# Kernel tuning notes

Hardware: AMD Instinct MI355X
Metric: run time of the kernel (lower is better)

Reference implementation:

```python
import jax, jax.numpy as jnp
import numpy as np
import math

B, S, H = 2, 1024, 768
NH = 12
DH = H // NH  # 64


def _heads(t):
    # (B,S,H) -> (B,NH,S,DH)
    b, s, _ = t.shape
    return t.reshape(b, s, NH, DH).transpose(0, 2, 1, 3)


def _merge(t):
    # (B,NH,S,DH) -> (B,S,H)
    b, nh, s, dh = t.shape
    return t.transpose(0, 2, 1, 3).reshape(b, s, nh * dh)


def _forward(x, y, vq_w, vq_b, vk_w, vk_b, vv_w, vv_b,
             dq_w, dq_b, dk_w, dk_b, dv_w, dv_b,
             van_fc_w, van_fc_b, WD_w, d_theta_w, d_theta_b, WV_w,
             diff_fc_w, diff_fc_b, v_gamma_w, v_gamma_b,
             diff_out_w, diff_out_b, van_out_w, van_out_b,
             diff_fus_w, diff_fus_b, van_fus_w, van_fus_b,
             gate_w, nf_w, nf_b, nf_out_w, final_w, final_b):
    scale = 1.0 / math.sqrt(DH)

    # ---- Vanilla attention (dropout is eval-mode identity) ----
    q = _heads(x @ vq_w + vq_b)
    k = _heads(y @ vk_w + vk_b)
    v = _heads(y @ vv_w + vv_b)
    scores = jnp.einsum('bhid,bhjd->bhij', q, k) * scale
    probs = jax.nn.softmax(scores, axis=-1)
    van_vector = _merge(jnp.einsum('bhij,bhjd->bhid', probs, v))

    # ---- Differential attention ----
    # scores[b,h,i,j] = sum_d (q[b,h,i,d] - k[b,h,i,d]) / sqrt(DH)  (constant over j,
    # due to the module's broadcast indexing). Keep explicit softmax for exact math/vjp.
    dq = _heads(x @ dq_w + dq_b)
    dk = _heads(y @ dk_w + dk_b)
    dv = _heads(y @ dv_w + dv_b)
    s_row = (dq.sum(-1) - dk.sum(-1)) * scale  # (B,NH,S)
    d_scores = jnp.broadcast_to(s_row[..., None], s_row.shape + (s_row.shape[-1],))
    d_probs = jax.nn.softmax(d_scores, axis=-1)
    diff_vector = _merge(jnp.einsum('bhij,bhjd->bhid', d_probs, dv))

    # ---- Coupled gating (SoftMax over dim=1 == sequence axis) ----
    theta = jnp.tanh(jnp.concatenate((diff_vector @ WD_w, x_lin(van_vector, van_fc_w, van_fc_b)), axis=-1))
    d_theta = diff_vector * jax.nn.softmax(theta @ d_theta_w + d_theta_b, axis=1)
    gamma = jnp.tanh(jnp.concatenate((van_vector @ WV_w, d_theta @ diff_fc_w + diff_fc_b), axis=-1))
    a_gamma = van_vector * jax.nn.softmax(gamma @ v_gamma_w + v_gamma_b, axis=1)
    diff_out = jnp.tanh(jnp.concatenate((diff_vector, d_theta), axis=-1) @ diff_out_w + diff_out_b)
    van_out = jnp.tanh(jnp.concatenate((van_vector, a_gamma), axis=-1) @ van_out_w + van_out_b)
    diff_fusion = jnp.tanh(diff_out @ diff_fus_w + diff_fus_b)
    van_fusion = jnp.tanh(van_out @ van_fus_w + van_fus_b)
    gate = jax.nn.sigmoid(jnp.concatenate((diff_fusion, van_fusion), axis=-1) @ gate_w)  # (B,S,1)
    fusion = gate * van_fusion + (1.0 - gate) * diff_fusion
    nf = jax.nn.sigmoid(jnp.concatenate((van_vector, fusion @ nf_w + nf_b), axis=-1) @ nf_out_w)
    return nf * jnp.tanh(fusion @ final_w + final_b)


def x_lin(t, w, b):
    return t @ w + b


def setup_inputs() -> dict:
    key = jax.random.key(0)
    ks = iter(jax.random.split(key, 64))
    def w(*shape):
        return jax.random.normal(next(ks), shape, jnp.float32) * 0.02
    def b(n):
        return jnp.zeros((n,), jnp.float32)
    inp = {
        'x': jax.random.normal(next(ks), (B, S, H), jnp.float32),
        'y': jax.random.normal(next(ks), (B, S, H), jnp.float32),
        'vq_w': w(H, H), 'vq_b': b(H), 'vk_w': w(H, H), 'vk_b': b(H), 'vv_w': w(H, H), 'vv_b': b(H),
        'dq_w': w(H, H), 'dq_b': b(H), 'dk_w': w(H, H), 'dk_b': b(H), 'dv_w': w(H, H), 'dv_b': b(H),
        'van_fc_w': w(H, H), 'van_fc_b': b(H),
        'WD_w': w(H, H),
        'd_theta_w': w(2 * H, H), 'd_theta_b': b(H),
        'WV_w': w(H, H),
        'diff_fc_w': w(H, H), 'diff_fc_b': b(H),
        'v_gamma_w': w(2 * H, H), 'v_gamma_b': b(H),
        'diff_out_w': w(2 * H, H), 'diff_out_b': b(H),
        'van_out_w': w(2 * H, H), 'van_out_b': b(H),
        'diff_fus_w': w(H, H), 'diff_fus_b': b(H),
        'van_fus_w': w(H, H), 'van_fus_b': b(H),
        'gate_w': w(2 * H, 1),
        'nf_w': w(H, H), 'nf_b': b(H),
        'nf_out_w': w(2 * H, 1),
        'final_w': w(H, H), 'final_b': b(H),
    }
    return inp


def reference(x, y, vq_w, vq_b, vk_w, vk_b, vv_w, vv_b,
              dq_w, dq_b, dk_w, dk_b, dv_w, dv_b,
              van_fc_w, van_fc_b, WD_w, d_theta_w, d_theta_b, WV_w,
              diff_fc_w, diff_fc_b, v_gamma_w, v_gamma_b,
              diff_out_w, diff_out_b, van_out_w, van_out_b,
              diff_fus_w, diff_fus_b, van_fus_w, van_fus_b,
              gate_w, nf_w, nf_b, nf_out_w, final_w, final_b):
    return _forward(x, y, vq_w, vq_b, vk_w, vk_b, vv_w, vv_b,
                    dq_w, dq_b, dk_w, dk_b, dv_w, dv_b,
                    van_fc_w, van_fc_b, WD_w, d_theta_w, d_theta_b, WV_w,
                    diff_fc_w, diff_fc_b, v_gamma_w, v_gamma_b,
                    diff_out_w, diff_out_b, van_out_w, van_out_b,
                    diff_fus_w, diff_fus_b, van_fus_w, van_fus_b,
                    gate_w, nf_w, nf_b, nf_out_w, final_w, final_b)
```

## Files before the change

### kernel.cpp

```cpp
#include <hip/hip_runtime.h>
#include <hip/hip_bf16.h>
#include <math.h>

#define H 768
#define S 1024
#define BATCH 2
#define T 2048
#define TH ((size_t)T * H)

typedef unsigned short u16;
typedef __attribute__((ext_vector_type(8))) short short8;
typedef __attribute__((ext_vector_type(4))) float f32x4;

__device__ __forceinline__ u16 f2b(float f) {
  __hip_bfloat16 h = __float2bfloat16(f);
  return *reinterpret_cast<u16*>(&h);
}
__device__ __forceinline__ float b2f(u16 u) {
  __hip_bfloat16 h = *reinterpret_cast<__hip_bfloat16*>(&u);
  return __bfloat162float(h);
}
__device__ __forceinline__ void gload16(const u16* g, u16* lds) {
  __builtin_amdgcn_global_load_lds((const __attribute__((address_space(1))) void*)g,
                                   (__attribute__((address_space(3))) void*)lds, 16, 0, 0);
}

__global__ __launch_bounds__(256) void cvt2_k(const float* __restrict__ X, const float* __restrict__ Y,
                                              u16* __restrict__ OX, u16* __restrict__ OY) {
  const float* src = blockIdx.y ? Y : X;
  u16* dst = blockIdx.y ? OY : OX;
  int i = blockIdx.x * 256 + threadIdx.x;
  float4 a = ((const float4*)src)[2 * i];
  float4 b = ((const float4*)src)[2 * i + 1];
  u16 tmp[8] = {f2b(a.x), f2b(a.y), f2b(a.z), f2b(a.w), f2b(b.x), f2b(b.y), f2b(b.z), f2b(b.w)};
  ((uint4*)dst)[i] = *(uint4*)tmp;
}

struct WprepArgs {
  const float* src[14];
  unsigned dst[14];
  int ktiles[14];
  int tstart[15];
};
__global__ __launch_bounds__(256) void wprep_k(WprepArgs a, u16* __restrict__ wt) {
  __shared__ float sT[64][68];
  int blk = blockIdx.x;
  int mi = 0;
  while (blk >= a.tstart[mi + 1]) ++mi;
  int local = blk - a.tstart[mi];
  int kt = a.ktiles[mi];
  int tn = local / kt, tk = local % kt;
  int K = kt * 64;
  const float* W = a.src[mi];
  u16* D = wt + a.dst[mi];
  int t = threadIdx.x;
  int r = t >> 2, c = (t & 3) * 16;
  const float4* srcp = (const float4*)(W + ((size_t)(tk * 64 + r)) * H + tn * 64 + c);
  float4 v0 = srcp[0], v1 = srcp[1], v2 = srcp[2], v3 = srcp[3];
  *(float4*)&sT[r][c] = v0; *(float4*)&sT[r][c + 4] = v1;
  *(float4*)&sT[r][c + 8] = v2; *(float4*)&sT[r][c + 12] = v3;
  __syncthreads();
  int n = t >> 2, kk = (t & 3) * 16;
  u16 tmp[16];
  #pragma unroll
  for (int j = 0; j < 16; ++j) tmp[j] = f2b(sT[kk + j][n]);
  uint4* dst = (uint4*)(D + ((size_t)(tn * 64 + n)) * K + tk * 64 + kk);
  dst[0] = *(uint4*)&tmp[0];
  dst[1] = *(uint4*)&tmp[8];
}

__global__ __launch_bounds__(256) void meany1_k(const float* __restrict__ Y, float* __restrict__ part) {
  int blk = blockIdx.x;
  int b = blk / 24, r = blk % 24, cc = r / 8, sc = r % 8;
  int c = cc * 256 + threadIdx.x;
  const float* yp = Y + (size_t)b * S * H + (size_t)sc * 128 * H + c;
  float s = 0.f;
  for (int j = 0; j < 128; ++j) s += yp[(size_t)j * H];
  part[(sc * 2 + b) * H + c] = s;
}
__global__ __launch_bounds__(256) void meany2_k(const float* __restrict__ part, float* __restrict__ ybar) {
  int t = blockIdx.x * 256 + threadIdx.x;
  float s = 0.f;
  int b = t / H, c = t % H;
  #pragma unroll
  for (int sc = 0; sc < 8; ++sc) s += part[(sc * 2 + b) * H + c];
  ybar[t] = s * (1.0f / 1024.0f);
}

__global__ __launch_bounds__(256) void gemv_k(const float* __restrict__ A, const float* __restrict__ W,
                                              const float* __restrict__ bias, float* __restrict__ O, int act) {
  int gid = blockIdx.x * 4 + (threadIdx.x >> 6);
  int lane = threadIdx.x & 63;
  int b = gid / H, n = gid % H;
  const float* a = A + b * H;
  float s = 0.f;
  #pragma unroll
  for (int i = 0; i < 12; ++i) {
    int k = lane + 64 * i;
    s = fmaf(a[k], W[(size_t)k * H + n], s);
  }
  #pragma unroll
  for (int off = 32; off; off >>= 1) s += __shfl_xor(s, off);
  if (lane == 0) {
    if (bias) s += bias[n];
    if (act) s = tanhf(s);
    O[gid] = s;
  }
}

struct Reg {
  const u16 *A, *W, *A2, *W2;
  const float *bias, *perbatch;
  u16* Cb; u16* CbT; float* Cf; float* colPart;
  int ldw, ldw2;
};
struct GArgs { Reg r0, r1, r2; int act; };

__global__ __launch_bounds__(256) void bgemm_k(GArgs ga) {
  __shared__ u16 sA[3][64 * 64];
  __shared__ u16 sB[3][64 * 64];
  int t = threadIdx.x;
  int ri = blockIdx.x / 12;
  Reg R;
  if (ri == 0) R = ga.r0; else if (ri == 1) R = ga.r1; else R = ga.r2;
  int n0 = (blockIdx.x % 12) * 64;
  int m0 = blockIdx.y * 64;
  int w = t >> 6, l = t & 63, lr = l & 15, lg = l >> 4;
  int wr = (w >> 1) * 32, wc = (w & 1) * 32;

  f32x4 acc[2][2];
  #pragma unroll
  for (int i = 0; i < 2; ++i)
    #pragma unroll
    for (int j = 0; j < 2; ++j) acc[i][j] = (f32x4){0.f, 0.f, 0.f, 0.f};

  int NT = R.A2 ? 24 : 12;

  auto stage = [&](int ti) {
    int bi = ti % 3;
    const u16* Aq = (ti < 12) ? R.A : R.A2;
    const u16* Wq = (ti < 12) ? R.W : R.W2;
    int ldwq = (ti < 12) ? R.ldw : R.ldw2;
    int k0 = (ti % 12) * 64;
    #pragma unroll
    for (int ii = 0; ii < 2; ++ii) {
      int chunk = w * 128 + ii * 64 + l;
      int rr = chunk >> 3, c8 = chunk & 7;
      gload16(Aq + (size_t)(m0 + rr) * H + k0 + 8 * (c8 ^ (rr & 7)), &sA[bi][0] + (w * 128 + ii * 64) * 8);
      gload16(Wq + (size_t)(n0 + rr) * ldwq + k0 + 8 * (c8 ^ (rr & 7)), &sB[bi][0] + (w * 128 + ii * 64) * 8);
    }
  };

  stage(0);
  stage(1);
  for (int kt = 0; kt < NT; ++kt) {
    if (kt + 1 < NT) asm volatile("s_waitcnt vmcnt(4)" ::: "memory");
    else             asm volatile("s_waitcnt vmcnt(0)" ::: "memory");
    __builtin_amdgcn_s_barrier();
    if (kt + 2 < NT) stage(kt + 2);
    const u16* sAv = &sA[kt % 3][0];
    const u16* sBv = &sB[kt % 3][0];
    #pragma unroll
    for (int kh = 0; kh < 2; ++kh) {
      short8 af[2], bfr[2];
      #pragma unroll
      for (int mi = 0; mi < 2; ++mi) {
        int row = wr + 16 * mi + lr;
        af[mi] = *(const short8*)(sAv + row * 64 + 8 * ((4 * kh + lg) ^ (row & 7)));
      }
      #pragma unroll
      for (int ni = 0; ni < 2; ++ni) {
        int row = wc + 16 * ni + lr;
        bfr[ni] = *(const short8*)(sBv + row * 64 + 8 * ((4 * kh + lg) ^ (row & 7)));
      }
      #pragma unroll
      for (int mi = 0; mi < 2; ++mi)
        #pragma unroll
        for (int ni = 0; ni < 2; ++ni)
          acc[mi][ni] = __builtin_amdgcn_mfma_f32_16x16x32_bf16(af[mi], bfr[ni], acc[mi][ni], 0, 0, 0);
    }
  }

  float ps[2] = {0.f, 0.f};
  #pragma unroll
  for (int mi = 0; mi < 2; ++mi) {
    #pragma unroll
    for (int ni = 0; ni < 2; ++ni) {
      int col = n0 + wc + 16 * ni + lr;
      u16 tmp4[4];
      #pragma unroll
      for (int reg = 0; reg < 4; ++reg) {
        int row = m0 + wr + 16 * mi + lg * 4 + reg;
        int bb = row >> 10;
        float v = acc[mi][ni][reg];
        if (R.bias) v += R.bias[col];
        if (R.perbatch) v += R.perbatch[bb * H + col];
        if (ga.act) v = tanhf(v);
        tmp4[reg] = f2b(v);
        if (R.Cb) R.Cb[(size_t)row * H + col] = tmp4[reg];
        if (R.Cf) R.Cf[(size_t)row * H + col] = v;
        if (R.colPart) ps[ni] += __expf(b2f(tmp4[reg]));
      }
      if (R.CbT) {
        int row0 = m0 + wr + 16 * mi + lg * 4;
        int bb = row0 >> 10, tok = row0 & 1023, hh = col >> 6, dd = col & 63;
        *(unsigned long long*)&R.CbT[((size_t)((bb * 12 + hh) * 64 + dd)) * 1024 + tok] =
            *(unsigned long long*)tmp4;
      }
    }
  }
  if (R.colPart) {
    #pragma unroll
    for (int ni = 0; ni < 2; ++ni) {
      float p = ps[ni];
      p += __shfl_xor(p, 16);
      p += __shfl_xor(p, 32);
      if (lg == 0) {
        int col = n0 + wc + 16 * ni + lr;
        R.colPart[(size_t)(blockIdx.y * 2 + (wr >> 5)) * H + col] = p;
      }
    }
  }
}

__global__ __launch_bounds__(256) void mattn_k(
    const u16* __restrict__ Q, const u16* __restrict__ Kg,
    const u16* __restrict__ VT, u16* __restrict__ O)
{
  __shared__ u16 sK[3][64 * 64];
  __shared__ u16 sV[3][64 * 64];
  __shared__ u16 sQ[64 * 64];
  __shared__ u16 sP[4 * 16 * 64];
  int t = threadIdx.x;
  int w = t >> 6, l = t & 63, lr = l & 15, lg = l >> 4;
  int blk = blockIdx.x;
  int b = blk / 192; int rem = blk % 192; int h = rem / 16; int q0 = (rem % 16) * 64;

  #pragma unroll
  for (int i = 0; i < 2; ++i) {
    int id = t + i * 256; int r = id >> 3, c = id & 7;
    uint4 v = *(const uint4*)(Q + ((size_t)(b * 1024 + q0 + r)) * H + h * 64 + 8 * c);
    *(uint4*)(&sQ[0] + r * 64 + 8 * (c ^ (r & 7))) = v;
  }
  asm volatile("s_waitcnt lgkmcnt(0)" ::: "memory");

  auto stageKV = [&](int ti) {
    int bi = ti % 3;
    int kv0 = ti * 64;
    #pragma unroll
    for (int ii = 0; ii < 2; ++ii) {
      int chunk = w * 128 + ii * 64 + l;
      int rr = chunk >> 3, c8 = chunk & 7;
      gload16(Kg + ((size_t)(b * 1024 + kv0 + rr)) * H + h * 64 + 8 * (c8 ^ (rr & 7)),
              &sK[bi][0] + (w * 128 + ii * 64) * 8);
      gload16(VT + ((size_t)((b * 12 + h) * 64 + rr)) * 1024 + kv0 + 8 * (c8 ^ (rr & 7)),
              &sV[bi][0] + (w * 128 + ii * 64) * 8);
    }
  };

  f32x4 oacc[4];
  #pragma unroll
  for (int i = 0; i < 4; ++i) oacc[i] = (f32x4){0.f, 0.f, 0.f, 0.f};
  float lsum[4] = {0.f, 0.f, 0.f, 0.f};

  stageKV(0);
  stageKV(1);

  for (int kt = 0; kt < 16; ++kt) {
    if (kt + 1 < 16) asm volatile("s_waitcnt vmcnt(4)" ::: "memory");
    else             asm volatile("s_waitcnt vmcnt(0)" ::: "memory");
    __builtin_amdgcn_s_barrier();
    if (kt + 2 < 16) stageKV(kt + 2);
    const u16* sKv = &sK[kt % 3][0];
    const u16* sVv = &sV[kt % 3][0];

    f32x4 sacc[4];
    #pragma unroll
    for (int i = 0; i < 4; ++i) sacc[i] = (f32x4){0.f, 0.f, 0.f, 0.f};
    #pragma unroll
    for (int kh = 0; kh < 2; ++kh) {
      int qrow = 16 * w + lr;
      short8 qf = *(const short8*)(&sQ[0] + qrow * 64 + 8 * ((4 * kh + lg) ^ (qrow & 7)));
      #pragma unroll
      for (int ns = 0; ns < 4; ++ns) {
        int krow = 16 * ns + lr;
        short8 kf = *(const short8*)(sKv + krow * 64 + 8 * ((4 * kh + lg) ^ (krow & 7)));
        sacc[ns] = __builtin_amdgcn_mfma_f32_16x16x32_bf16(qf, kf, sacc[ns], 0, 0, 0);
      }
    }

    #pragma unroll
    for (int r = 0; r < 4; ++r) {
      int q = lg * 4 + r;
      #pragma unroll
      for (int ns = 0; ns < 4; ++ns) {
        float p = __expf(sacc[ns][r] * 0.125f);
        lsum[r] += p;
        int kv = 16 * ns + lr;
        unsigned byteoff = (unsigned)(w * 2048 + q * 128 + ((kv * 2) ^ ((q & 7) << 4)));
        *(u16*)((char*)sP + byteoff) = f2b(p);
      }
    }

    #pragma unroll
    for (int kh = 0; kh < 2; ++kh) {
      short8 pf = *(const short8*)((char*)sP + w * 2048 + lr * 128 + (((4 * kh + lg) << 4) ^ ((lr & 7) << 4)));
      #pragma unroll
      for (int ds = 0; ds < 4; ++ds) {
        int vrow = 16 * ds + lr;
        short8 vf = *(const short8*)(sVv + vrow * 64 + 8 * ((4 * kh + lg) ^ (vrow & 7)));
        oacc[ds] = __builtin_amdgcn_mfma_f32_16x16x32_bf16(pf, vf, oacc[ds], 0, 0, 0);
      }
    }
  }

  #pragma unroll
  for (int r = 0; r < 4; ++r) {
    #pragma unroll
    for (int off = 1; off < 16; off <<= 1) lsum[r] += __shfl_xor(lsum[r], off);
    float inv = 1.0f / lsum[r];
    int qrow = q0 + 16 * w + lg * 4 + r;
    #pragma unroll
    for (int ds = 0; ds < 4; ++ds) {
      int d = 16 * ds + lr;
      O[((size_t)(b * 1024 + qrow)) * H + h * 64 + d] = f2b(oacc[ds][r] * inv);
    }
  }
}

__global__ __launch_bounds__(256) void colsmA_k(
    const u16* __restrict__ Z, const float* __restrict__ part,
    const float* __restrict__ mulvec, const u16* __restrict__ mulmat, u16* __restrict__ O) {
  int blk = blockIdx.x;
  int b = blk >> 7, sc = blk & 127;
  int t = threadIdx.x;
  float s0 = 0.f, s1 = 0.f, s2 = 0.f;
  for (int i = b * 32; i < b * 32 + 32; ++i) {
    const float* pp = part + (size_t)i * H;
    s0 += pp[t]; s1 += pp[t + 256]; s2 += pp[t + 512];
  }
  float i0 = 1.0f / s0, i1 = 1.0f / s1, i2 = 1.0f / s2;
  size_t base = ((size_t)(b * 1024 + sc * 8)) * H;
  float m0 = 0.f, m1 = 0.f, m2 = 0.f;
  if (mulvec) { m0 = mulvec[b * H + t]; m1 = mulvec[b * H + t + 256]; m2 = mulvec[b * H + t + 512]; }
  #pragma unroll
  for (int j = 0; j < 8; ++j) {
    size_t row = base + (size_t)j * H;
    float e0 = __expf(b2f(Z[row + t]));
    float e1 = __expf(b2f(Z[row + t + 256]));
    float e2 = __expf(b2f(Z[row + t + 512]));
    float u0 = mulmat ? b2f(mulmat[row + t]) : m0;
    float u1 = mulmat ? b2f(mulmat[row + t + 256]) : m1;
    float u2 = mulmat ? b2f(mulmat[row + t + 512]) : m2;
    O[row + t] = f2b(u0 * e0 * i0);
    O[row + t + 256] = f2b(u1 * e1 * i1);
    O[row + t + 512] = f2b(u2 * e2 * i2);
  }
}

__global__ __launch_bounds__(256) void gatefuse_k(
    const u16* __restrict__ DF, const u16* __restrict__ VF,
    const float* __restrict__ GW, u16* __restrict__ FU)
{
  __shared__ float red[256];
  int tok = blockIdx.x;
  int t = threadIdx.x;
  const u16* df = DF + (size_t)tok * H;
  const u16* vf = VF + (size_t)tok * H;
  float dv[3], vv[3];
  float p = 0.f;
  #pragma unroll
  for (int i = 0; i < 3; ++i) {
    int c = t + i * 256;
    dv[i] = b2f(df[c]); vv[i] = b2f(vf[c]);
    p = fmaf(dv[i], GW[c], p);
    p = fmaf(vv[i], GW[H + c], p);
  }
  red[t] = p; __syncthreads();
  for (int st = 128; st; st >>= 1) { if (t < st) red[t] += red[t + st]; __syncthreads(); }
  float g = 1.0f / (1.0f + __expf(-red[0]));
  u16* fu = FU + (size_t)tok * H;
  #pragma unroll
  for (int i = 0; i < 3; ++i) {
    int c = t + i * 256;
    fu[c] = f2b(g * vv[i] + (1.0f - g) * dv[i]);
  }
}

__global__ __launch_bounds__(256) void nffinal_k(
    const u16* __restrict__ VAN, const float* __restrict__ NP,
    const float* __restrict__ NW, const float* __restrict__ FP,
    float* __restrict__ OUT)
{
  __shared__ float red[256];
  int tok = blockIdx.x;
  int t = threadIdx.x;
  const u16* va = VAN + (size_t)tok * H;
  const float* np = NP + (size_t)tok * H;
  float p = 0.f;
  #pragma unroll
  for (int i = 0; i < 3; ++i) {
    int c = t + i * 256;
    p = fmaf(b2f(va[c]), NW[c], p);
    p = fmaf(np[c], NW[H + c], p);
  }
  red[t] = p; __syncthreads();
  for (int st = 128; st; st >>= 1) { if (t < st) red[t] += red[t + st]; __syncthreads(); }
  float nf = 1.0f / (1.0f + __expf(-red[0]));
  const float* fp = FP + (size_t)tok * H;
  float* o = OUT + (size_t)tok * H;
  #pragma unroll
  for (int i = 0; i < 3; ++i) {
    int c = t + i * 256;
    o[c] = nf * tanhf(fp[c]);
  }
}

extern "C" void kernel_launch(void* const* d_in, const int* in_sizes, int n_in,
                              void* d_out, int out_size, void* d_ws, size_t ws_size,
                              hipStream_t stream) {
  const float* x        = (const float*)d_in[0];
  const float* y        = (const float*)d_in[1];
  const float* vq_w     = (const float*)d_in[2];
  const float* vq_b     = (const float*)d_in[3];
  const float* vk_w     = (const float*)d_in[4];
  const float* vk_b     = (const float*)d_in[5];
  const float* vv_w     = (const float*)d_in[6];
  const float* vv_b     = (const float*)d_in[7];
  const float* dv_w     = (const float*)d_in[12];
  const float* dv_b     = (const float*)d_in[13];
  const float* van_fc_w = (const float*)d_in[14];
  const float* van_fc_b = (const float*)d_in[15];
  const float* d_theta_w= (const float*)d_in[17];
  const float* WV_w     = (const float*)d_in[19];
  const float* diff_fc_w= (const float*)d_in[20];
  const float* diff_fc_b= (const float*)d_in[21];
  const float* v_gamma_w= (const float*)d_in[22];
  const float* diff_out_w=(const float*)d_in[24];
  const float* diff_out_b=(const float*)d_in[25];
  const float* van_out_w= (const float*)d_in[26];
  const float* van_out_b= (const float*)d_in[27];
  const float* diff_fus_w=(const float*)d_in[28];
  const float* diff_fus_b=(const float*)d_in[29];
  const float* van_fus_w= (const float*)d_in[30];
  const float* van_fus_b= (const float*)d_in[31];
  const float* gate_w   = (const float*)d_in[32];
  const float* nf_w     = (const float*)d_in[33];
  const float* nf_b     = (const float*)d_in[34];
  const float* nf_out_w = (const float*)d_in[35];
  const float* final_w  = (const float*)d_in[36];
  const float* final_b  = (const float*)d_in[37];
  float* out = (float*)d_out;

  u16* wt = (u16*)d_ws;
  const size_t HH_ = (size_t)H * H;
  const size_t HH2 = 2 * HH_;
  size_t woff[14];
  const float* wsrc[14] = {vq_w, vk_w, vv_w, van_fc_w, WV_w, diff_fc_w, diff_fus_w, van_fus_w,
                           nf_w, final_w, d_theta_w, v_gamma_w, diff_out_w, van_out_w};
  int wk[14] = {12,12,12,12,12,12,12,12,12,12, 24,24,24,24};
  size_t o = 0;
  for (int i = 0; i < 14; ++i) { woff[i] = o; o += (i < 10) ? HH_ : HH2; }
  u16* bufs = wt + o;
  u16* bX   = bufs + 0 * TH;
  u16* bY   = bufs + 1 * TH;
  u16* bQ   = bufs + 2 * TH;
  u16* bK   = bufs + 3 * TH;
  u16* bV   = bufs + 4 * TH;
  u16* bVT  = bufs + 5 * TH;
  u16* bVan = bufs + 6 * TH;
  float* F0 = (float*)(bufs + 7 * TH);
  float* F1 = F0 + TH;
  float* sm = F1 + TH;
  float* ybar  = sm;
  float* dvbar = sm + 1536;
  float* c2    = sm + 3072;
  float* part  = sm + 4608;
  float* colp  = sm + 4608 + 12288;

  WprepArgs wa;
  int ts = 0;
  for (int i = 0; i < 14; ++i) {
    wa.src[i] = wsrc[i];
    wa.dst[i] = (unsigned)woff[i];
    wa.ktiles[i] = wk[i];
    wa.tstart[i] = ts;
    ts += wk[i] * 12;
  }
  wa.tstart[14] = ts;
  wprep_k<<<ts, 256, 0, stream>>>(wa, wt);
  cvt2_k<<<dim3(TH / 8 / 256, 2), 256, 0, stream>>>(x, y, bX, bY);

  meany1_k<<<48, 256, 0, stream>>>(y, part);
  meany2_k<<<6, 256, 0, stream>>>(part, ybar);
  gemv_k<<<384, 256, 0, stream>>>(ybar, dv_w, dv_b, dvbar, 0);
  gemv_k<<<384, 256, 0, stream>>>(dvbar, diff_out_w, diff_out_b, c2, 0);

  const u16 *wt_vq = wt + woff[0], *wt_vk = wt + woff[1], *wt_vv = wt + woff[2],
            *wt_vanfc = wt + woff[3], *wt_WV = wt + woff[4], *wt_difffc = wt + woff[5],
            *wt_difffus = wt + woff[6], *wt_vanfus = wt + woff[7], *wt_nf = wt + woff[8],
            *wt_final = wt + woff[9], *wt_dtheta = wt + woff[10], *wt_vg = wt + woff[11],
            *wt_diffout = wt + woff[12], *wt_vanout = wt + woff[13];
  #define NO nullptr
  Reg RZ = {NO, NO, NO, NO, NO, NO, NO, NO, NO, NO, 0, 0};

  {
    GArgs g;
    g.r0 = {bX, wt_vq, NO, NO, vq_b, NO, bQ, NO, NO, NO, H, 0};
    g.r1 = {bY, wt_vk, NO, NO, vk_b, NO, bK, NO, NO, NO, H, 0};
    g.r2 = {bY, wt_vv, NO, NO, vv_b, NO, NO, bVT, NO, NO, H, 0};
    g.act = 0;
    bgemm_k<<<dim3(36, 32), 256, 0, stream>>>(g);
  }
  mattn_k<<<384, 256, 0, stream>>>(bQ, bK, bVT, bVan);

  {
    GArgs g;
    g.r0 = {bVan, wt_vanfc, NO, NO, van_fc_b, NO, bX, NO, NO, NO, H, 0};
    g.r1 = {bVan, wt_WV, NO, NO, NO, NO, bK, NO, NO, NO, H, 0};
    g.r2 = RZ;
    g.act = 1;
    bgemm_k<<<dim3(24, 32), 256, 0, stream>>>(g);
  }
  {
    GArgs g;
    g.r0 = {bX, wt_dtheta + H, NO, NO, NO, NO, bY, NO, NO, colp, 2 * H, 0};
    g.r1 = RZ; g.r2 = RZ;
    g.act = 0;
    bgemm_k<<<dim3(12, 32), 256, 0, stream>>>(g);
  }
  colsmA_k<<<256, 256, 0, stream>>>(bY, colp, dvbar, NO, bQ);
  {
    GArgs g;
    g.r0 = {bQ, wt_difffc, NO, NO, diff_fc_b, NO, bV, NO, NO, NO, H, 0};
    g.r1 = {bQ, wt_diffout + H, NO, NO, NO, c2, bY, NO, NO, NO, 2 * H, 0};
    g.r2 = RZ;
    g.act = 1;
    bgemm_k<<<dim3(24, 32), 256, 0, stream>>>(g);
  }
  {
    GArgs g;
    g.r0 = {bK, wt_vg, bV, wt_vg + H, NO, NO, bX, NO, NO, colp, 2 * H, 2 * H};
    g.r1 = RZ; g.r2 = RZ;
    g.act = 0;
    bgemm_k<<<dim3(12, 32), 256, 0, stream>>>(g);
  }
  colsmA_k<<<256, 256, 0, stream>>>(bX, colp, NO, bVan, bX);
  {
    GArgs g;
    g.r0 = {bVan, wt_vanout, bX, wt_vanout + H, van_out_b, NO, bK, NO, NO, NO, 2 * H, 2 * H};
    g.r1 = {bY, wt_difffus, NO, NO, diff_fus_b, NO, bQ, NO, NO, NO, H, 0};
    g.r2 = RZ;
    g.act = 1;
    bgemm_k<<<dim3(24, 32), 256, 0, stream>>>(g);
  }
  {
    GArgs g;
    g.r0 = {bK, wt_vanfus, NO, NO, van_fus_b, NO, bV, NO, NO, NO, H, 0};
    g.r1 = RZ; g.r2 = RZ;
    g.act = 1;
    bgemm_k<<<dim3(12, 32), 256, 0, stream>>>(g);
  }
  gatefuse_k<<<T, 256, 0, stream>>>(bQ, bV, gate_w, bY);
  {
    GArgs g;
    g.r0 = {bY, wt_nf, NO, NO, nf_b, NO, NO, NO, F0, NO, H, 0};
    g.r1 = {bY, wt_final, NO, NO, final_b, NO, NO, NO, F1, NO, H, 0};
    g.r2 = RZ;
    g.act = 0;
    bgemm_k<<<dim3(24, 32), 256, 0, stream>>>(g);
  }
  nffinal_k<<<T, 256, 0, stream>>>(bVan, F0, nf_out_w, F1, out);
}
```

Baseline: 232.9 us.

## Use 8 waves per GEMM block and keep Q fragments in registers in attention

The batched GEMM kernel moves from 4 waves (each computing a 32x32 subtile) to 8 waves (each computing a 16x32 subtile) per 64x64 output tile. Each thread now issues one async load per operand per stage, and the vmcnt waits and per-block column-partial indexing are adjusted to match, with colsm reading 64 partial rows per batch. This raises waves per block to hide latency, at the cost of less register-level reuse of B fragments. Separately, the attention kernel loads its Q fragments into registers once, after the KV prefetch is issued, instead of rereading them from LDS on every KV tile.

Result: faster. 226.3 us (-2.8%).

```diff
diff --git a/kernel.cpp b/kernel.cpp
--- a/kernel.cpp
+++ b/kernel.cpp
@@ -116,7 +116,7 @@
 };
 struct GArgs { Reg r0, r1, r2; int act; };
 
-__global__ __launch_bounds__(256) void bgemm_k(GArgs ga) {
+__global__ __launch_bounds__(512) void bgemm_k(GArgs ga) {
   __shared__ u16 sA[3][64 * 64];
   __shared__ u16 sB[3][64 * 64];
   int t = threadIdx.x;
@@ -126,13 +126,11 @@
   int n0 = (blockIdx.x % 12) * 64;
   int m0 = blockIdx.y * 64;
   int w = t >> 6, l = t & 63, lr = l & 15, lg = l >> 4;
-  int wr = (w >> 1) * 32, wc = (w & 1) * 32;
-
-  f32x4 acc[2][2];
-  #pragma unroll
-  for (int i = 0; i < 2; ++i)
-    #pragma unroll
-    for (int j = 0; j < 2; ++j) acc[i][j] = (f32x4){0.f, 0.f, 0.f, 0.f};
+  int wr = (w & 3) * 16, wc = (w >> 2) * 32;
+
+  f32x4 acc[2];
+  acc[0] = (f32x4){0.f, 0.f, 0.f, 0.f};
+  acc[1] = (f32x4){0.f, 0.f, 0.f, 0.f};
 
   int NT = R.A2 ? 24 : 12;
 
@@ -142,19 +140,15 @@
     const u16* Wq = (ti < 12) ? R.W : R.W2;
     int ldwq = (ti < 12) ? R.ldw : R.ldw2;
     int k0 = (ti % 12) * 64;
-    #pragma unroll
-    for (int ii = 0; ii < 2; ++ii) {
-      int chunk = w * 128 + ii * 64 + l;
-      int rr = chunk >> 3, c8 = chunk & 7;
-      gload16(Aq + (size_t)(m0 + rr) * H + k0 + 8 * (c8 ^ (rr & 7)), &sA[bi][0] + (w * 128 + ii * 64) * 8);
-      gload16(Wq + (size_t)(n0 + rr) * ldwq + k0 + 8 * (c8 ^ (rr & 7)), &sB[bi][0] + (w * 128 + ii * 64) * 8);
-    }
+    int rr = t >> 3, c8 = t & 7;
+    gload16(Aq + (size_t)(m0 + rr) * H + k0 + 8 * (c8 ^ (rr & 7)), &sA[bi][0] + t * 8);
+    gload16(Wq + (size_t)(n0 + rr) * ldwq + k0 + 8 * (c8 ^ (rr & 7)), &sB[bi][0] + t * 8);
   };
 
   stage(0);
   stage(1);
   for (int kt = 0; kt < NT; ++kt) {
-    if (kt + 1 < NT) asm volatile("s_waitcnt vmcnt(4)" ::: "memory");
+    if (kt + 1 < NT) asm volatile("s_waitcnt vmcnt(2)" ::: "memory");
     else             asm volatile("s_waitcnt vmcnt(0)" ::: "memory");
     __builtin_amdgcn_s_barrier();
     if (kt + 2 < NT) stage(kt + 2);
@@ -162,51 +156,40 @@
     const u16* sBv = &sB[kt % 3][0];
     #pragma unroll
     for (int kh = 0; kh < 2; ++kh) {
-      short8 af[2], bfr[2];
-      #pragma unroll
-      for (int mi = 0; mi < 2; ++mi) {
-        int row = wr + 16 * mi + lr;
-        af[mi] = *(const short8*)(sAv + row * 64 + 8 * ((4 * kh + lg) ^ (row & 7)));
-      }
+      int arow = wr + lr;
+      short8 af = *(const short8*)(sAv + arow * 64 + 8 * ((4 * kh + lg) ^ (arow & 7)));
       #pragma unroll
       for (int ni = 0; ni < 2; ++ni) {
-        int row = wc + 16 * ni + lr;
-        bfr[ni] = *(const short8*)(sBv + row * 64 + 8 * ((4 * kh + lg) ^ (row & 7)));
+        int brow = wc + 16 * ni + lr;
+        short8 bf = *(const short8*)(sBv + brow * 64 + 8 * ((4 * kh + lg) ^ (brow & 7)));
+        acc[ni] = __builtin_amdgcn_mfma_f32_16x16x32_bf16(af, bf, acc[ni], 0, 0, 0);
       }
-      #pragma unroll
-      for (int mi = 0; mi < 2; ++mi)
-        #pragma unroll
-        for (int ni = 0; ni < 2; ++ni)
-          acc[mi][ni] = __builtin_amdgcn_mfma_f32_16x16x32_bf16(af[mi], bfr[ni], acc[mi][ni], 0, 0, 0);
     }
   }
 
   float ps[2] = {0.f, 0.f};
   #pragma unroll
-  for (int mi = 0; mi < 2; ++mi) {
-    #pragma unroll
-    for (int ni = 0; ni < 2; ++ni) {
-      int col = n0 + wc + 16 * ni + lr;
-      u16 tmp4[4];
-      #pragma unroll
-      for (int reg = 0; reg < 4; ++reg) {
-        int row = m0 + wr + 16 * mi + lg * 4 + reg;
-        int bb = row >> 10;
-        float v = acc[mi][ni][reg];
-        if (R.bias) v += R.bias[col];
-        if (R.perbatch) v += R.perbatch[bb * H + col];
-        if (ga.act) v = tanhf(v);
-        tmp4[reg] = f2b(v);
-        if (R.Cb) R.Cb[(size_t)row * H + col] = tmp4[reg];
-        if (R.Cf) R.Cf[(size_t)row * H + col] = v;
-        if (R.colPart) ps[ni] += __expf(b2f(tmp4[reg]));
-      }
-      if (R.CbT) {
-        int row0 = m0 + wr + 16 * mi + lg * 4;
-        int bb = row0 >> 10, tok = row0 & 1023, hh = col >> 6, dd = col & 63;
-        *(unsigned long long*)&R.CbT[((size_t)((bb * 12 + hh) * 64 + dd)) * 1024 + tok] =
-            *(unsigned long long*)tmp4;
-      }
+  for (int ni = 0; ni < 2; ++ni) {
+    int col = n0 + wc + 16 * ni + lr;
+    u16 tmp4[4];
+    #pragma unroll
+    for (int reg = 0; reg < 4; ++reg) {
+      int row = m0 + wr + lg * 4 + reg;
+      int bb = row >> 10;
+      float v = acc[ni][reg];
+      if (R.bias) v += R.bias[col];
+      if (R.perbatch) v += R.perbatch[bb * H + col];
+      if (ga.act) v = tanhf(v);
+      tmp4[reg] = f2b(v);
+      if (R.Cb) R.Cb[(size_t)row * H + col] = tmp4[reg];
+      if (R.Cf) R.Cf[(size_t)row * H + col] = v;
+      if (R.colPart) ps[ni] += __expf(b2f(tmp4[reg]));
+    }
+    if (R.CbT) {
+      int row0 = m0 + wr + lg * 4;
+      int bb = row0 >> 10, tok = row0 & 1023, hh = col >> 6, dd = col & 63;
+      *(unsigned long long*)&R.CbT[((size_t)((bb * 12 + hh) * 64 + dd)) * 1024 + tok] =
+          *(unsigned long long*)tmp4;
     }
   }
   if (R.colPart) {
@@ -217,7 +200,7 @@
       p += __shfl_xor(p, 32);
       if (lg == 0) {
         int col = n0 + wc + 16 * ni + lr;
-        R.colPart[(size_t)(blockIdx.y * 2 + (wr >> 5)) * H + col] = p;
+        R.colPart[(size_t)(blockIdx.y * 4 + (w & 3)) * H + col] = p;
       }
     }
   }
@@ -242,7 +225,6 @@
     uint4 v = *(const uint4*)(Q + ((size_t)(b * 1024 + q0 + r)) * H + h * 64 + 8 * c);
     *(uint4*)(&sQ[0] + r * 64 + 8 * (c ^ (r & 7))) = v;
   }
-  asm volatile("s_waitcnt lgkmcnt(0)" ::: "memory");
 
   auto stageKV = [&](int ti) {
     int bi = ti % 3;
@@ -258,13 +240,21 @@
     }
   };
 
+  stageKV(0);
+  stageKV(1);
+  asm volatile("s_waitcnt lgkmcnt(0)" ::: "memory");
+  __builtin_amdgcn_s_barrier();
+  short8 qreg[2];
+  #pragma unroll
+  for (int kh = 0; kh < 2; ++kh) {
+    int qrow = 16 * w + lr;
+    qreg[kh] = *(const short8*)(&sQ[0] + qrow * 64 + 8 * ((4 * kh + lg) ^ (qrow & 7)));
+  }
+
   f32x4 oacc[4];
   #pragma unroll
   for (int i = 0; i < 4; ++i) oacc[i] = (f32x4){0.f, 0.f, 0.f, 0.f};
   float lsum[4] = {0.f, 0.f, 0.f, 0.f};
-
-  stageKV(0);
-  stageKV(1);
 
   for (int kt = 0; kt < 16; ++kt) {
     if (kt + 1 < 16) asm volatile("s_waitcnt vmcnt(4)" ::: "memory");
@@ -279,13 +269,11 @@
     for (int i = 0; i < 4; ++i) sacc[i] = (f32x4){0.f, 0.f, 0.f, 0.f};
     #pragma unroll
     for (int kh = 0; kh < 2; ++kh) {
-      int qrow = 16 * w + lr;
-      short8 qf = *(const short8*)(&sQ[0] + qrow * 64 + 8 * ((4 * kh + lg) ^ (qrow & 7)));
       #pragma unroll
       for (int ns = 0; ns < 4; ++ns) {
         int krow = 16 * ns + lr;
         short8 kf = *(const short8*)(sKv + krow * 64 + 8 * ((4 * kh + lg) ^ (krow & 7)));
-        sacc[ns] = __builtin_amdgcn_mfma_f32_16x16x32_bf16(qf, kf, sacc[ns], 0, 0, 0);
+        sacc[ns] = __builtin_amdgcn_mfma_f32_16x16x32_bf16(qreg[kh], kf, sacc[ns], 0, 0, 0);
       }
     }
 
@@ -335,7 +323,7 @@
   int b = blk >> 7, sc = blk & 127;
   int t = threadIdx.x;
   float s0 = 0.f, s1 = 0.f, s2 = 0.f;
-  for (int i = b * 32; i < b * 32 + 32; ++i) {
+  for (int i = b * 64; i < b * 64 + 64; ++i) {
     const float* pp = part + (size_t)i * H;
     s0 += pp[t]; s1 += pp[t + 256]; s2 += pp[t + 512];
   }
@@ -510,7 +498,7 @@
     g.r1 = {bY, wt_vk, NO, NO, vk_b, NO, bK, NO, NO, NO, H, 0};
     g.r2 = {bY, wt_vv, NO, NO, vv_b, NO, NO, bVT, NO, NO, H, 0};
     g.act = 0;
-    bgemm_k<<<dim3(36, 32), 256, 0, stream>>>(g);
+    bgemm_k<<<dim3(36, 32), 512, 0, stream>>>(g);
   }
   mattn_k<<<384, 256, 0, stream>>>(bQ, bK, bVT, bVan);
 
@@ -520,14 +508,14 @@
     g.r1 = {bVan, wt_WV, NO, NO, NO, NO, bK, NO, NO, NO, H, 0};
     g.r2 = RZ;
     g.act = 1;
-    bgemm_k<<<dim3(24, 32), 256, 0, stream>>>(g);
+    bgemm_k<<<dim3(24, 32), 512, 0, stream>>>(g);
   }
   {
     GArgs g;
     g.r0 = {bX, wt_dtheta + H, NO, NO, NO, NO, bY, NO, NO, colp, 2 * H, 0};
     g.r1 = RZ; g.r2 = RZ;
     g.act = 0;
-    bgemm_k<<<dim3(12, 32), 256, 0, stream>>>(g);
+    bgemm_k<<<dim3(12, 32), 512, 0, stream>>>(g);
   }
   colsmA_k<<<256, 256, 0, stream>>>(bY, colp, dvbar, NO, bQ);
   {
@@ -536,14 +524,14 @@
     g.r1 = {bQ, wt_diffout + H, NO, NO, NO, c2, bY, NO, NO, NO, 2 * H, 0};
     g.r2 = RZ;
     g.act = 1;
-    bgemm_k<<<dim3(24, 32), 256, 0, stream>>>(g);
+    bgemm_k<<<dim3(24, 32), 512, 0, stream>>>(g);
   }
   {
     GArgs g;
     g.r0 = {bK, wt_vg, bV, wt_vg + H, NO, NO, bX, NO, NO, colp, 2 * H, 2 * H};
     g.r1 = RZ; g.r2 = RZ;
     g.act = 0;
-    bgemm_k<<<dim3(12, 32), 256, 0, stream>>>(g);
+    bgemm_k<<<dim3(12, 32), 512, 0, stream>>>(g);
   }
   colsmA_k<<<256, 256, 0, stream>>>(bX, colp, NO, bVan, bX);
   {
@@ -552,14 +540,14 @@
     g.r1 = {bY, wt_difffus, NO, NO, diff_fus_b, NO, bQ, NO, NO, NO, H, 0};
     g.r2 = RZ;
     g.act = 1;
-    bgemm_k<<<dim3(24, 32), 256, 0, stream>>>(g);
+    bgemm_k<<<dim3(24, 32), 512, 0, stream>>>(g);
   }
   {
     GArgs g;
     g.r0 = {bK, wt_vanfus, NO, NO, van_fus_b, NO, bV, NO, NO, NO, H, 0};
     g.r1 = RZ; g.r2 = RZ;
     g.act = 1;
-    bgemm_k<<<dim3(12, 32), 256, 0, stream>>>(g);
+    bgemm_k<<<dim3(12, 32), 512, 0, stream>>>(g);
   }
   gatefuse_k<<<T, 256, 0, stream>>>(bQ, bV, gate_w, bY);
   {
@@ -568,7 +556,7 @@
     g.r1 = {bY, wt_final, NO, NO, final_b, NO, NO, NO, F1, NO, H, 0};
     g.r2 = RZ;
     g.act = 0;
-    bgemm_k<<<dim3(24, 32), 256, 0, stream>>>(g);
+    bgemm_k<<<dim3(24, 32), 512, 0, stream>>>(g);
   }
   nffinal_k<<<T, 256, 0, stream>>>(bVan, F0, nf_out_w, F1, out);
 }
```
